# Kernel optimization log

Hardware: AMD Instinct MI355X
Metric: run time of the kernel (lower is better)

The kernel has to match this reference:

```python
import jax, jax.numpy as jnp
import numpy as np

N, E, G = 50000, 800000, 64
IN, HID, T, EDGE_DIM, HLS = 32, 64, 2, 2, 32
# deg histogram: all nodes degree 16 -> avg_deg['log'] = log(16+1)
AVG_LOG = float(np.log(17.0))


def _pna(x, src, dst, eattr, We, be, Wpre, bpre, Wpost, bpost, Wlin, blin):
    """PNAConv with aggregators [mean,min,max,std], scalers [identity,amp,att],
    towers=T, pre_layers=1, post_layers=1, divide_input=False."""
    n, F = x.shape
    enc = eattr @ We + be                                   # [E, F] edge encoder
    # message: concat(x_i, x_j, edge) -> per-tower Linear(3F -> F)
    h = jnp.concatenate([x[dst], x[src], enc], axis=-1)     # [E, 3F] (same for all towers)
    m = jnp.einsum('ef,tfo->eto', h, Wpre) + bpre           # [E, T, F]
    ones = jnp.ones((m.shape[0],), m.dtype)
    cnt = jax.ops.segment_sum(ones, dst, num_segments=n)    # in-degree [N]
    d = jnp.maximum(cnt, 1.0)[:, None, None]
    s = jax.ops.segment_sum(m, dst, num_segments=n)
    mean = s / d
    msq = jax.ops.segment_sum(m * m, dst, num_segments=n) / d
    std = jnp.sqrt(jax.nn.relu(msq - mean * mean) + 1e-5)
    has = (cnt > 0)[:, None, None]
    mn = jnp.where(has, jax.ops.segment_min(m, dst, num_segments=n), 0.0)
    mx = jnp.where(has, jax.ops.segment_max(m, dst, num_segments=n), 0.0)
    agg = jnp.concatenate([mean, mn, mx, std], axis=-1)     # [N, T, 4F]
    logd = jnp.log(d + 1.0)
    scaled = jnp.concatenate([agg, agg * (logd / AVG_LOG), agg * (AVG_LOG / logd)], axis=-1)  # [N,T,12F]
    xt = jnp.broadcast_to(x[:, None, :], (n, Wpre.shape[0], F))
    out = jnp.concatenate([xt, scaled], axis=-1)            # [N, T, 13F]
    o = jnp.einsum('nti,tio->nto', out, Wpost) + bpost      # [N, T, F_out]
    return o.reshape(n, -1) @ Wlin + blin                   # [N, HID]


def setup_inputs():
    key = jax.random.key(0)
    ks = iter(jax.random.split(key, 48))
    def p(shape):
        return jax.random.normal(next(ks), shape, jnp.float32) * 0.05
    inp = {}
    inp['x'] = jax.random.normal(next(ks), (N, IN), jnp.float32)
    inp['edge_attr'] = jax.random.normal(next(ks), (E, EDGE_DIM), jnp.float32)
    inp['hls_attr'] = jax.random.normal(next(ks), (G, HLS), jnp.float32)
    inp['edge_index'] = jax.random.randint(next(ks), (2, E), 0, N)
    inp['batch'] = jnp.sort(jax.random.randint(next(ks), (N,), 0, G))
    Fo = HID // T
    for l, Fin in enumerate([IN, HID]):
        inp[f'We{l}'] = p((EDGE_DIM, Fin)); inp[f'be{l}'] = jnp.zeros((Fin,), jnp.float32)
        inp[f'Wpre{l}'] = p((T, 3 * Fin, Fin)); inp[f'bpre{l}'] = jnp.zeros((T, Fin), jnp.float32)
        inp[f'Wpost{l}'] = p((T, 13 * Fin, Fo)); inp[f'bpost{l}'] = jnp.zeros((T, Fo), jnp.float32)
        inp[f'Wlin{l}'] = p((HID, HID)); inp[f'blin{l}'] = jnp.zeros((HID,), jnp.float32)
    inp['W1'] = p((HID + HLS, 64)); inp['b1'] = jnp.zeros((64,), jnp.float32)
    inp['W2'] = p((64, 64)); inp['b2'] = jnp.zeros((64,), jnp.float32)
    inp['W3'] = p((64, 1)); inp['b3'] = jnp.zeros((1,), jnp.float32)
    return inp


def reference(x, edge_attr, hls_attr,
              We0, be0, Wpre0, bpre0, Wpost0, bpost0, Wlin0, blin0,
              We1, be1, Wpre1, bpre1, Wpost1, bpost1, Wlin1, blin1,
              W1, b1, W2, b2, W3, b3,
              edge_index, batch):
    src, dst = edge_index[0], edge_index[1]
    h = jax.nn.relu(_pna(x, src, dst, edge_attr, We0, be0, Wpre0, bpre0, Wpost0, bpost0, Wlin0, blin0))
    h = jax.nn.relu(_pna(h, src, dst, edge_attr, We1, be1, Wpre1, bpre1, Wpost1, bpost1, Wlin1, blin1))
    g = jax.ops.segment_sum(h, batch, num_segments=G)       # global_add_pool [G, HID]
    g = jnp.concatenate([g, hls_attr], axis=-1)
    g = jax.nn.relu(g @ W1 + b1)
    g = jax.nn.relu(g @ W2 + b2)
    return g @ W3 + b3                                      # [G, 1]
```

## Files before the change

### kernel.cpp

```cpp
#include <hip/hip_runtime.h>
#include <math.h>
#include <float.h>

#define NN 50000
#define EE 800000
#define CAP 64

#define NB 196
#define SPAN 256
#define BCAP 4608

typedef unsigned short ushort_t;
typedef short short8 __attribute__((ext_vector_type(8)));
typedef float floatx4 __attribute__((ext_vector_type(4)));

__device__ __constant__ float kAVG_LOG = 2.8332133440562162f;

__device__ inline ushort_t f2bf(float v) {
    union { float f; unsigned u; } x; x.f = v;
    unsigned r = x.u + 0x7fffu + ((x.u >> 16) & 1u);
    return (ushort_t)(r >> 16);
}
__device__ inline float bf2f(ushort_t b) {
    union { unsigned u; float f; } x; x.u = ((unsigned)b) << 16; return x.f;
}
__device__ inline float bitsf(unsigned u) {
    union { unsigned u; float f; } x; x.u = u; return x.f;
}
__device__ inline void splitbf(float v, ushort_t& hi, ushort_t& lo) {
    hi = f2bf(v);
    lo = f2bf(v - bf2f(hi));
}

template <int F>
__device__ void prep_ab_dev(const float* __restrict__ We, const float* __restrict__ be,
                            const float* __restrict__ Wpre, const float* __restrict__ bpre,
                            float* __restrict__ U, float* __restrict__ Wab,
                            float* __restrict__ bias_ab) {
    const int TF = 2 * F;
    int tid = threadIdx.x;
    for (int idx = tid; idx < 2 * TF; idx += 1024) {
        int c = idx / TF, f = idx % TF;
        int t = f / F, o = f % F;
        float s = 0.f;
        for (int g = 0; g < F; ++g)
            s += We[c * F + g] * Wpre[((size_t)t * 3 * F + 2 * F + g) * F + o];
        U[idx] = s;
    }
    for (int idx = tid; idx < F * 2 * TF; idx += 1024) {
        int g = idx / (2 * TF), cc = idx % (2 * TF);
        int t, o, row;
        if (cc < TF) { t = cc / F; o = cc % F; row = g; }
        else { int c2 = cc - TF; t = c2 / F; o = c2 % F; row = F + g; }
        Wab[idx] = Wpre[((size_t)t * 3 * F + row) * F + o];
    }
    for (int cc = tid; cc < 2 * TF; cc += 1024) {
        float v = 0.f;
        if (cc < TF) {
            int t = cc / F, o = cc % F;
            float s = 0.f;
            for (int g = 0; g < F; ++g)
                s += be[g] * Wpre[((size_t)t * 3 * F + 2 * F + g) * F + o];
            v = s + bpre[t * F + o];
        }
        bias_ab[cc] = v;
    }
}

template <int F>
__device__ void prep_zf_elem(int idx, const float* __restrict__ Wpost, const float* __restrict__ Wlin,
                             ushort_t* __restrict__ Bh, ushort_t* __restrict__ Bl) {
    const int KT = 9 * F;
    int jg = idx / KT, k = idx - jg * KT;
    int b = jg >> 6, j = jg & 63;
    float v = 0.f;
    if (k < F) {
        if (b == 0) {
#pragma unroll
            for (int t = 0; t < 2; ++t)
#pragma unroll
                for (int c = 0; c < 32; ++c)
                    v += Wpost[((size_t)t * 13 * F + k) * 32 + c] * Wlin[(t * 32 + c) * 64 + j];
        }
    } else {
        int r = k - F;
        int t = r / (4 * F), rr = r - t * 4 * F;
#pragma unroll
        for (int c = 0; c < 32; ++c)
            v += Wpost[((size_t)t * 13 * F + F + b * 4 * F + rr) * 32 + c] * Wlin[(t * 32 + c) * 64 + j];
    }
    ushort_t h_, l_;
    splitbf(v, h_, l_);
    Bh[(size_t)jg * KT + k] = h_;
    Bl[(size_t)jg * KT + k] = l_;
}

#define PARTB 196
#define PZ0B  54
#define PZ1B  108
#define PINITB 1563

__global__ __launch_bounds__(1024) void prep_part_init(
    const int* __restrict__ ei, const float* __restrict__ ea,
    int* __restrict__ gcount, uint2* __restrict__ part,
    const float* We0, const float* be0, const float* Wpre0, const float* bpre0,
    const float* Wpost0, const float* Wlin0, const float* bpost0, const float* blin0,
    const float* We1, const float* be1, const float* Wpre1, const float* bpre1,
    const float* Wpost1, const float* Wlin1, const float* bpost1, const float* blin1,
    float* U0, float* Wab0, float* bias_ab0, ushort_t* Bh0, ushort_t* Bl0, float* bias_zf0,
    float* U1, float* Wab1, float* bias_ab1, ushort_t* Bh1, ushort_t* Bl1, float* bias_zf1,
    const float* __restrict__ x, ushort_t* __restrict__ xb) {
    __shared__ int hist[NB];
    __shared__ int lbase[NB];
    int tid = threadIdx.x;
    int b = blockIdx.x;
    if (b < PARTB) {
        int e0 = b * 4096;
        for (int i = tid; i < NB; i += 1024) hist[i] = 0;
        __syncthreads();
        int bq[4], rnk[4];
        unsigned px[4], py[4];
#pragma unroll
        for (int q = 0; q < 4; ++q) {
            int e = e0 + q * 1024 + tid;
            bq[q] = -1;
            if (e < EE) {
                int s = ei[e];
                int d = ei[EE + e];
                float2 v = *(const float2*)(ea + 2 * e);
                bq[q] = d >> 8;
                px[q] = ((unsigned)(d & 255) << 16) | (unsigned)s;
                py[q] = ((unsigned)f2bf(v.y) << 16) | (unsigned)f2bf(v.x);
                rnk[q] = atomicAdd(&hist[bq[q]], 1);
            }
        }
        __syncthreads();
        for (int i = tid; i < NB; i += 1024)
            lbase[i] = atomicAdd(&gcount[i], hist[i]);
        __syncthreads();
#pragma unroll
        for (int q = 0; q < 4; ++q) {
            if (bq[q] >= 0) {
                int slot = lbase[bq[q]] + rnk[q];
                if (slot < BCAP)
                    part[(size_t)bq[q] * BCAP + slot] = make_uint2(px[q], py[q]);
            }
        }
        return;
    }
    b -= PARTB;
    if (b < PZ0B) {
        prep_zf_elem<32>(b * 1024 + tid, Wpost0, Wlin0, Bh0, Bl0);
    } else if (b < PZ0B + PZ1B) {
        prep_zf_elem<64>((b - PZ0B) * 1024 + tid, Wpost1, Wlin1, Bh1, Bl1);
    } else if (b == PZ0B + PZ1B) {
        prep_ab_dev<32>(We0, be0, Wpre0, bpre0, U0, Wab0, bias_ab0);
    } else if (b == PZ0B + PZ1B + 1) {
        prep_ab_dev<64>(We1, be1, Wpre1, bpre1, U1, Wab1, bias_ab1);
    } else if (b == PZ0B + PZ1B + 2) {
        for (int j = tid; j < 64; j += 1024) {
            float s0 = blin0[j], s1 = blin1[j];
#pragma unroll
            for (int t = 0; t < 2; ++t)
#pragma unroll
                for (int c = 0; c < 32; ++c) {
                    s0 += bpost0[t * 32 + c] * Wlin0[(t * 32 + c) * 64 + j];
                    s1 += bpost1[t * 32 + c] * Wlin1[(t * 32 + c) * 64 + j];
                }
            bias_zf0[j] = s0;
            bias_zf1[j] = s1;
        }
    } else {
        int i = (b - (PZ0B + PZ1B + 3)) * 1024 + tid;
        if (i < NN * 32) xb[i] = f2bf(x[i]);
    }
}

__device__ void csr_fill_block(int g, const int* __restrict__ gcount,
                               const uint2* __restrict__ part,
                               int* __restrict__ cnt, uint2* __restrict__ csr) {
    __shared__ int lcnt[SPAN];
    int tid = threadIdx.x;
    lcnt[tid] = 0;
    __syncthreads();
    int total = gcount[g];
    if (total > BCAP) total = BCAP;
    size_t pbase = (size_t)g * BCAP;
    for (int i = tid; i < total; i += 256) {
        uint2 rec = part[pbase + i];
        int rel = rec.x >> 16;
        int src = rec.x & 0xffff;
        int p = atomicAdd(&lcnt[rel], 1);
        if (p < CAP) {
            int node = (g << 8) + rel;
            csr[(size_t)node * CAP + p] = make_uint2((unsigned)src, rec.y);
        }
    }
    __syncthreads();
    int node = (g << 8) + tid;
    if (node < NN) cnt[node] = lcnt[tid];
}

__device__ void gemm_bias_block(const float* __restrict__ A, const float* __restrict__ B,
                                const float* __restrict__ bias, float* __restrict__ Ca,
                                ushort_t* __restrict__ Cb, int M, int K, int Ncols, int bstart,
                                int mb, int cb) {
    __shared__ float As[32][132];
    __shared__ float Bs[32][68];
    int m0 = mb * 128, c0 = cb * 64;
    int tid = threadIdx.x;
    int tx = tid & 15, ty = tid >> 4;
    int ms = tid >> 3, u = tid & 7;
    float acc[8][4] = {};
    for (int k0 = 0; k0 < K; k0 += 32) {
#pragma unroll
        for (int p = 0; p < 4; ++p) {
            int m = ms + 32 * p;
            int gm = m0 + m;
            float4 v = make_float4(0.f, 0.f, 0.f, 0.f);
            if (gm < M) v = *(const float4*)(A + (size_t)gm * K + k0 + u * 4);
            As[u * 4 + 0][m] = v.x; As[u * 4 + 1][m] = v.y;
            As[u * 4 + 2][m] = v.z; As[u * 4 + 3][m] = v.w;
        }
#pragma unroll
        for (int p = 0; p < 2; ++p) {
            int idx = tid + 256 * p;
            int kk = idx >> 4, q = idx & 15;
            *(float4*)&Bs[kk][q * 4] = *(const float4*)(B + (size_t)(k0 + kk) * Ncols + c0 + q * 4);
        }
        __syncthreads();
#pragma unroll 8
        for (int k = 0; k < 32; ++k) {
            float a0[8], b0[4];
            *(float4*)&a0[0] = *(const float4*)&As[k][ty * 8];
            *(float4*)&a0[4] = *(const float4*)&As[k][ty * 8 + 4];
            *(float4*)&b0[0] = *(const float4*)&Bs[k][tx * 4];
#pragma unroll
            for (int i = 0; i < 8; ++i)
#pragma unroll
                for (int j = 0; j < 4; ++j) acc[i][j] = fmaf(a0[i], b0[j], acc[i][j]);
        }
        __syncthreads();
    }
    float bj[4];
#pragma unroll
    for (int j = 0; j < 4; ++j) bj[j] = bias[c0 + tx * 4 + j];
    bool bside = (c0 >= bstart);
    int TFw = bstart;
#pragma unroll
    for (int i = 0; i < 8; ++i) {
        int gm = m0 + ty * 8 + i;
        if (gm >= M) continue;
        float v0 = acc[i][0] + bj[0], v1 = acc[i][1] + bj[1];
        float v2 = acc[i][2] + bj[2], v3 = acc[i][3] + bj[3];
        if (!bside) {
            *(float4*)(Ca + (size_t)gm * TFw + c0 + tx * 4) = make_float4(v0, v1, v2, v3);
        } else {
            ushort4 w;
            w.x = f2bf(v0); w.y = f2bf(v1); w.z = f2bf(v2); w.w = f2bf(v3);
            *(ushort4*)(Cb + (size_t)gm * TFw + (c0 - bstart) + tx * 4) = w;
        }
    }
}

__global__ __launch_bounds__(256) void gemm_bias(const float* __restrict__ A, const float* __restrict__ B,
                                                 const float* __restrict__ bias, float* __restrict__ Ca,
                                                 ushort_t* __restrict__ Cb, int M, int K, int Ncols, int bstart) {
    gemm_bias_block(A, B, bias, Ca, Cb, M, K, Ncols, bstart, blockIdx.x, blockIdx.y);
}

__global__ __launch_bounds__(256) void csr_gemm0(
    const int* __restrict__ gcount, const uint2* __restrict__ part,
    int* __restrict__ cnt, uint2* __restrict__ csr,
    const float* __restrict__ A, const float* __restrict__ B, const float* __restrict__ bias,
    float* __restrict__ Ca, ushort_t* __restrict__ Cb) {
    int bx = blockIdx.x;
    if (bx % 5 == 0) {
        csr_fill_block(bx / 5, gcount, part, cnt, csr);
    } else {
        int idx = bx - 1 - bx / 5;
        gemm_bias_block(A, B, bias, Ca, Cb, NN, 32, 128, 64, idx % 391, idx / 391);
    }
}

template <int F>
__global__ __launch_bounds__(256) void aggregate(const float* __restrict__ ABa, const ushort_t* __restrict__ ABb,
                                                 const int* __restrict__ cnt, const uint2* __restrict__ csr,
                                                 const float* __restrict__ U,
                                                 ushort_t* __restrict__ agg_b, float2* __restrict__ sc) {
    const int TF = 2 * F;
    const int FPL = TF / 64;
    int lane = threadIdx.x & 63;
    int n = blockIdx.x * 4 + (threadIdx.x >> 6);
    if (n >= NN) return;
    n = __builtin_amdgcn_readfirstlane(n);
    int f0 = FPL * lane;

    float base[FPL], u0[FPL], u1[FPL], sum[FPL], sq[FPL], mn[FPL], mx[FPL];
#pragma unroll
    for (int r = 0; r < FPL; ++r) {
        base[r] = ABa[(size_t)n * TF + f0 + r];
        u0[r] = U[f0 + r];
        u1[r] = U[TF + f0 + r];
        sum[r] = 0.f; sq[r] = 0.f; mn[r] = FLT_MAX; mx[r] = -FLT_MAX;
    }
    int deg = cnt[n];
    int ec = deg < CAP ? deg : CAP;
    const uint2* __restrict__ p = csr + (size_t)n * CAP;

    auto body = [&](unsigned epi, unsigned wvi) {
        float ex = bitsf(epi << 16);
        float ey = bitsf(epi & 0xffff0000u);
        float v[FPL];
        if constexpr (FPL == 2) {
            v[0] = bitsf(wvi << 16);
            v[1] = bitsf(wvi & 0xffff0000u);
        } else {
            v[0] = bitsf(wvi << 16);
        }
#pragma unroll
        for (int r = 0; r < FPL; ++r) {
            float q = fmaf(ex, u0[r], fmaf(ey, u1[r], v[r]));
            sum[r] += q;
            sq[r] = fmaf(q, q, sq[r]);
            mn[r] = fminf(mn[r], q);
            mx[r] = fmaxf(mx[r], q);
        }
    };

    for (int e0 = 0; e0 < ec; e0 += 16) {
        uint4 c[8];
#pragma unroll
        for (int j = 0; j < 8; ++j) c[j] = *(const uint4*)(p + e0 + 2 * j);
        unsigned sb[16], ep[16];
#pragma unroll
        for (int j = 0; j < 8; ++j) {
            sb[2 * j] = c[j].x;     ep[2 * j] = c[j].y;
            sb[2 * j + 1] = c[j].z; ep[2 * j + 1] = c[j].w;
        }
        int rem = ec - e0;
        unsigned wv[16];
        if (rem >= 16) {
#pragma unroll
            for (int i = 0; i < 16; ++i) {
                const ushort_t* row = ABb + (size_t)sb[i] * TF;
                if constexpr (FPL == 2) wv[i] = *(const unsigned*)(row + f0);
                else wv[i] = row[f0];
            }
#pragma unroll
            for (int i = 0; i < 16; ++i) body(ep[i], wv[i]);
        } else {
#pragma unroll
            for (int i = 0; i < 16; ++i) {
                if (i < rem) {
                    const ushort_t* row = ABb + (size_t)sb[i] * TF;
                    if constexpr (FPL == 2) wv[i] = *(const unsigned*)(row + f0);
                    else wv[i] = row[f0];
                }
            }
#pragma unroll
            for (int i = 0; i < 16; ++i)
                if (i < rem) body(ep[i], wv[i]);
        }
    }

    float d = (float)(deg > 1 ? deg : 1);
    float inv_d = 1.f / d;
    bool has = deg > 0;
#pragma unroll
    for (int r = 0; r < FPL; ++r) {
        float mean_q = sum[r] * inv_d;
        float var = sq[r] * inv_d - mean_q * mean_q;
        float stdv = sqrtf(fmaxf(var, 0.f) + 1e-5f);
        float mean = has ? base[r] + mean_q : 0.f;
        float vmn = has ? base[r] + mn[r] : 0.f;
        float vmx = has ? base[r] + mx[r] : 0.f;
        int f = f0 + r;
        int t = f / F, o = f - t * F;
        size_t rowb = (size_t)n * (4 * TF) + (size_t)t * (4 * F);
        agg_b[rowb + o] = f2bf(mean);
        agg_b[rowb + F + o] = f2bf(vmn);
        agg_b[rowb + 2 * F + o] = f2bf(vmx);
        agg_b[rowb + 3 * F + o] = f2bf(stdv);
    }
    if (lane == 0) {
        float logd = logf(d + 1.f);
        sc[n] = make_float2(logd / kAVG_LOG, kAVG_LOG / logd);
    }
}

template <int F, bool POOL>
__global__ __launch_bounds__(512, 2) void gemm_zf(
    const ushort_t* __restrict__ xs_b, const ushort_t* __restrict__ agg_b,
    const ushort_t* __restrict__ Bh, const ushort_t* __restrict__ Bl,
    const float* __restrict__ bias_zf, const float2* __restrict__ sc,
    float* __restrict__ H, ushort_t* __restrict__ H_b,
    const int* __restrict__ batch, float* __restrict__ pool) {
    const int KT = 9 * F;
    extern __shared__ char smem[];
    ushort_t* A_s  = (ushort_t*)smem;
    ushort_t* Bh_s = A_s + 128 * 40;
    ushort_t* Bl_s = Bh_s + 192 * 40;
    float* hbuf = (float*)smem;

    int m0 = blockIdx.x * 128;
    int tid = threadIdx.x;
    int lane = tid & 63;
    int wave = tid >> 6;
    int wr = wave >> 2;
    int wc = wave & 3;
    int ln = lane & 15, quad = lane >> 4;

    floatx4 acc[4][3];
#pragma unroll
    for (int i = 0; i < 4; ++i)
#pragma unroll
        for (int j = 0; j < 3; ++j) acc[i][j] = (floatx4)(0.f);

    int arow = tid >> 2, asg = tid & 3;
    int bcol[2], bsg[2];
    bool bok[2];
#pragma unroll
    for (int p = 0; p < 2; ++p) {
        int idx = tid + 512 * p;
        bok[p] = idx < 768;
        bcol[p] = idx >> 2;
        bsg[p] = idx & 3;
    }

    const short8 zero8 = {0, 0, 0, 0, 0, 0, 0, 0};
    short8 pa, pbh[2], pbl[2];
    {
        int c0 = asg * 8;
        int gm = m0 + arow;
        pa = zero8;
        if (gm < NN) pa = *(const short8*)(xs_b + (size_t)gm * F + c0);
#pragma unroll
        for (int p = 0; p < 2; ++p) {
            pbh[p] = zero8; pbl[p] = zero8;
            if (bok[p]) {
                pbh[p] = *(const short8*)(Bh + (size_t)bcol[p] * KT + bsg[p] * 8);
                pbl[p] = *(const short8*)(Bl + (size_t)bcol[p] * KT + bsg[p] * 8);
            }
        }
    }

    for (int k0 = 0; k0 < KT; k0 += 32) {
        *(short8*)&A_s[arow * 40 + asg * 8] = pa;
#pragma unroll
        for (int p = 0; p < 2; ++p) {
            if (bok[p]) {
                *(short8*)&Bh_s[bcol[p] * 40 + bsg[p] * 8] = pbh[p];
                *(short8*)&Bl_s[bcol[p] * 40 + bsg[p] * 8] = pbl[p];
            }
        }
        __syncthreads();
        short8 bh[3], bl[3];
#pragma unroll
        for (int b = 0; b < 3; ++b) {
            int col = b * 64 + wc * 16 + ln;
            bh[b] = *(short8*)&Bh_s[col * 40 + quad * 8];
            bl[b] = *(short8*)&Bl_s[col * 40 + quad * 8];
        }
        int kn = k0 + 32;
        if (kn < KT) {
            int c0 = kn + asg * 8;
            int gm = m0 + arow;
            pa = zero8;
            if (gm < NN) {
                pa = (c0 < F) ? *(const short8*)(xs_b + (size_t)gm * F + c0)
                              : *(const short8*)(agg_b + (size_t)gm * 8 * F + (c0 - F));
            }
#pragma unroll
            for (int p = 0; p < 2; ++p) {
                if (bok[p]) {
                    pbh[p] = *(const short8*)(Bh + (size_t)bcol[p] * KT + kn + bsg[p] * 8);
                    pbl[p] = *(const short8*)(Bl + (size_t)bcol[p] * KT + kn + bsg[p] * 8);
                }
            }
        }
#pragma unroll
        for (int rf = 0; rf < 4; ++rf) {
            short8 ah = *(short8*)&A_s[((wr * 4 + rf) * 16 + ln) * 40 + quad * 8];
#pragma unroll
            for (int b = 0; b < 3; ++b) {
                acc[rf][b] = __builtin_amdgcn_mfma_f32_16x16x32_bf16(ah, bh[b], acc[rf][b], 0, 0, 0);
                acc[rf][b] = __builtin_amdgcn_mfma_f32_16x16x32_bf16(ah, bl[b], acc[rf][b], 0, 0, 0);
            }
        }
        __syncthreads();
    }

    int ocol = wc * 16 + ln;
    float bcolv = bias_zf[ocol];

    if (POOL) __syncthreads();

#pragma unroll
    for (int rf = 0; rf < 4; ++rf) {
#pragma unroll
        for (int reg = 0; reg < 4; ++reg) {
            int r = (wr * 4 + rf) * 16 + quad * 4 + reg;
            int gm = m0 + r;
            float2 s = make_float2(0.f, 0.f);
            if (gm < NN) s = sc[gm];
            float y = acc[rf][0][reg] + s.x * acc[rf][1][reg] + s.y * acc[rf][2][reg] + bcolv;
            y = fmaxf(y, 0.f);
            if (POOL) {
                hbuf[r * 68 + ocol] = (gm < NN) ? y : 0.f;
            } else if (gm < NN) {
                H[(size_t)gm * 64 + ocol] = y;
                H_b[(size_t)gm * 64 + ocol] = f2bf(y);
            }
        }
    }
    if (POOL) {
        __syncthreads();
        int col = tid & 63, grp = tid >> 6;
        float a = 0.f;
        int cur = -1;
        for (int i = 0; i < 16; ++i) {
            int r = grp * 16 + i;
            int gm = m0 + r;
            if (gm >= NN) break;
            int b = batch[gm];
            if (b != cur) {
                if (cur >= 0) atomicAdd(&pool[cur * 64 + col], a);
                cur = b; a = 0.f;
            }
            a += hbuf[r * 68 + col];
        }
        if (cur >= 0) atomicAdd(&pool[cur * 64 + col], a);
    }
}

__global__ __launch_bounds__(256) void head_kernel(const float* __restrict__ gpool, const float* __restrict__ hls,
                                                   const float* __restrict__ W1, const float* __restrict__ b1,
                                                   const float* __restrict__ W2, const float* __restrict__ b2,
                                                   const float* __restrict__ W3, const float* __restrict__ b3,
                                                   float* __restrict__ out) {
    __shared__ float gin[64][96];
    __shared__ float r1[64][64];
    __shared__ float r2[64][64];
    int tid = threadIdx.x;
    for (int idx = tid; idx < 64 * 96; idx += 256) {
        int g = idx / 96, j = idx % 96;
        gin[g][j] = (j < 64) ? gpool[g * 64 + j] : hls[g * 32 + (j - 64)];
    }
    __syncthreads();
    for (int idx = tid; idx < 64 * 64; idx += 256) {
        int g = idx / 64, j = idx % 64;
        float acc = b1[j];
        for (int k = 0; k < 96; ++k) acc = fmaf(gin[g][k], W1[k * 64 + j], acc);
        r1[g][j] = fmaxf(acc, 0.f);
    }
    __syncthreads();
    for (int idx = tid; idx < 64 * 64; idx += 256) {
        int g = idx / 64, j = idx % 64;
        float acc = b2[j];
        for (int k = 0; k < 64; ++k) acc = fmaf(r1[g][k], W2[k * 64 + j], acc);
        r2[g][j] = fmaxf(acc, 0.f);
    }
    __syncthreads();
    if (tid < 64) {
        float acc = b3[0];
        for (int k = 0; k < 64; ++k) acc = fmaf(r2[tid][k], W3[k], acc);
        out[tid] = acc;
    }
}

extern "C" void kernel_launch(void* const* d_in, const int* in_sizes, int n_in,
                              void* d_out, int out_size, void* d_ws, size_t ws_size,
                              hipStream_t stream) {
    (void)in_sizes; (void)n_in; (void)out_size; (void)ws_size;
    const float* x     = (const float*)d_in[0];
    const float* eattr = (const float*)d_in[1];
    const float* hls   = (const float*)d_in[2];
    const int*   eidx  = (const int*)d_in[3];
    const int*   batch = (const int*)d_in[4];
    const float* We[2]    = {(const float*)d_in[5],  (const float*)d_in[13]};
    const float* be[2]    = {(const float*)d_in[6],  (const float*)d_in[14]};
    const float* Wpre[2]  = {(const float*)d_in[7],  (const float*)d_in[15]};
    const float* bpre[2]  = {(const float*)d_in[8],  (const float*)d_in[16]};
    const float* Wpost[2] = {(const float*)d_in[9],  (const float*)d_in[17]};
    const float* bpost[2] = {(const float*)d_in[10], (const float*)d_in[18]};
    const float* Wlin[2]  = {(const float*)d_in[11], (const float*)d_in[19]};
    const float* blin[2]  = {(const float*)d_in[12], (const float*)d_in[20]};
    const float* W1 = (const float*)d_in[21]; const float* b1 = (const float*)d_in[22];
    const float* W2 = (const float*)d_in[23]; const float* b2 = (const float*)d_in[24];
    const float* W3 = (const float*)d_in[25]; const float* b3 = (const float*)d_in[26];
    float* out = (float*)d_out;

    char* ws = (char*)d_ws;
    size_t off = 0;
    auto carve = [&](size_t bytes) -> char* {
        char* p = ws + off;
        off = (off + bytes + 255) & ~(size_t)255;
        return p;
    };
    int*      cnt      = (int*)carve((size_t)NN * 4);
    uint2*    csr      = (uint2*)carve((size_t)NN * CAP * 8);
    float*    ABa      = (float*)carve((size_t)NN * 128 * 4);
    ushort_t* ABb      = (ushort_t*)carve((size_t)NN * 128 * 2);
    ushort_t* agg_b    = (ushort_t*)carve((size_t)NN * 512 * 2);
    float2*   sc       = (float2*)carve((size_t)NN * 8);
    ushort_t* xs_b     = (ushort_t*)carve((size_t)NN * 32 * 2);
    float*    h1       = (float*)carve((size_t)NN * 64 * 4);
    ushort_t* h1_b     = (ushort_t*)carve((size_t)NN * 64 * 2);
    float*    U0       = (float*)carve(256 * 4);
    float*    U1       = (float*)carve(256 * 4);
    float*    Wab0     = (float*)carve(16384 * 4);
    float*    Wab1     = (float*)carve(16384 * 4);
    float*    bias_ab0 = (float*)carve(256 * 4);
    float*    bias_ab1 = (float*)carve(256 * 4);
    ushort_t* Bh0      = (ushort_t*)carve((size_t)192 * 288 * 2);
    ushort_t* Bl0      = (ushort_t*)carve((size_t)192 * 288 * 2);
    ushort_t* Bh1      = (ushort_t*)carve((size_t)192 * 576 * 2);
    ushort_t* Bl1      = (ushort_t*)carve((size_t)192 * 576 * 2);
    float*    bias_zf0 = (float*)carve(64 * 4);
    float*    bias_zf1 = (float*)carve(64 * 4);
    float*    pool     = (float*)carve(64 * 64 * 4);
    int*      gcount   = (int*)carve(NB * 4);
    uint2*    part     = (uint2*)agg_b;

    const int MB128 = (NN + 127) / 128;
    const int SMEM_ZF = (128 * 40 + 192 * 40 + 192 * 40) * 2;
    const int FUSEDB = NB + MB128 * 2;
    const int MERGEDB = PARTB + PZ0B + PZ1B + 3 + PINITB;

    hipMemsetAsync(gcount, 0, NB * 4, stream);
    hipMemsetAsync(pool, 0, 64 * 64 * 4, stream);

    prep_part_init<<<MERGEDB, 1024, 0, stream>>>(
        eidx, eattr, gcount, part,
        We[0], be[0], Wpre[0], bpre[0], Wpost[0], Wlin[0], bpost[0], blin[0],
        We[1], be[1], Wpre[1], bpre[1], Wpost[1], Wlin[1], bpost[1], blin[1],
        U0, Wab0, bias_ab0, Bh0, Bl0, bias_zf0,
        U1, Wab1, bias_ab1, Bh1, Bl1, bias_zf1,
        x, xs_b);

    csr_gemm0<<<FUSEDB, 256, 0, stream>>>(gcount, part, cnt, csr, x, Wab0, bias_ab0, ABa, ABb);
    aggregate<32><<<(NN + 3) / 4, 256, 0, stream>>>(ABa, ABb, cnt, csr, U0, agg_b, sc);
    gemm_zf<32, false><<<MB128, 512, SMEM_ZF, stream>>>(xs_b, agg_b, Bh0, Bl0, bias_zf0, sc,
                                                        h1, h1_b, batch, pool);

    gemm_bias<<<dim3(MB128, 4), 256, 0, stream>>>(h1, Wab1, bias_ab1, ABa, ABb, NN, 64, 256, 128);
    aggregate<64><<<(NN + 3) / 4, 256, 0, stream>>>(ABa, ABb, cnt, csr, U1, agg_b, sc);
    gemm_zf<64, true><<<MB128, 512, SMEM_ZF, stream>>>(h1_b, agg_b, Bh1, Bl1, bias_zf1, sc,
                                                       nullptr, nullptr, batch, pool);

    head_kernel<<<1, 256, 0, stream>>>(pool, hls, W1, b1, W2, b2, W3, b3, out);
}
```

Before: 321.5 us.

## Fuse neighbor aggregation into the post-GEMM kernel per 128-row tile

Removes the standalone aggregate kernel launches. Each 512-thread GEMM block now first aggregates its own 128 nodes, one wave per node over 16 passes, writing agg_b and sc. It then syncs and runs the existing post-transform GEMM on those rows. This saves a launch and kernel boundary per layer and may keep the aggregated rows in cache, but aggregation now runs at the GEMM kernel's lower grid size and occupancy (launch_bounds 512,2), which can reduce latency hiding for the irregular gathers.

```diff
diff --git a/kernel.cpp b/kernel.cpp
--- a/kernel.cpp
+++ b/kernel.cpp
@@ -284,15 +284,13 @@
 }
 
 template <int F>
-__global__ __launch_bounds__(256) void aggregate(const float* __restrict__ ABa, const ushort_t* __restrict__ ABb,
-                                                 const int* __restrict__ cnt, const uint2* __restrict__ csr,
-                                                 const float* __restrict__ U,
-                                                 ushort_t* __restrict__ agg_b, float2* __restrict__ sc) {
+__device__ void agg_node(int n, int lane,
+                         const float* __restrict__ ABa, const ushort_t* __restrict__ ABb,
+                         const int* __restrict__ cnt, const uint2* __restrict__ csr,
+                         const float* __restrict__ U,
+                         ushort_t* agg_b, float2* sc) {
     const int TF = 2 * F;
     const int FPL = TF / 64;
-    int lane = threadIdx.x & 63;
-    int n = blockIdx.x * 4 + (threadIdx.x >> 6);
-    if (n >= NN) return;
     n = __builtin_amdgcn_readfirstlane(n);
     int f0 = FPL * lane;
 
@@ -390,10 +388,13 @@
 }
 
 template <int F, bool POOL>
-__global__ __launch_bounds__(512, 2) void gemm_zf(
-    const ushort_t* __restrict__ xs_b, const ushort_t* __restrict__ agg_b,
+__global__ __launch_bounds__(512, 2) void aggzf(
+    const float* __restrict__ ABa, const ushort_t* __restrict__ ABb,
+    const int* __restrict__ cnt, const uint2* __restrict__ csr,
+    const float* __restrict__ U,
+    const ushort_t* __restrict__ xs_b, ushort_t* agg_b,
     const ushort_t* __restrict__ Bh, const ushort_t* __restrict__ Bl,
-    const float* __restrict__ bias_zf, const float2* __restrict__ sc,
+    const float* __restrict__ bias_zf, float2* sc,
     float* __restrict__ H, ushort_t* __restrict__ H_b,
     const int* __restrict__ batch, float* __restrict__ pool) {
     const int KT = 9 * F;
@@ -407,6 +408,15 @@
     int tid = threadIdx.x;
     int lane = tid & 63;
     int wave = tid >> 6;
+
+#pragma unroll 1
+    for (int pss = 0; pss < 16; ++pss) {
+        int n = m0 + pss * 8 + wave;
+        if (n < NN)
+            agg_node<F>(n, lane, ABa, ABb, cnt, csr, U, agg_b, sc);
+    }
+    __syncthreads();
+
     int wr = wave >> 2;
     int wc = wave & 3;
     int ln = lane & 15, quad = lane >> 4;
@@ -640,14 +650,14 @@
         x, xs_b);
 
     csr_gemm0<<<FUSEDB, 256, 0, stream>>>(gcount, part, cnt, csr, x, Wab0, bias_ab0, ABa, ABb);
-    aggregate<32><<<(NN + 3) / 4, 256, 0, stream>>>(ABa, ABb, cnt, csr, U0, agg_b, sc);
-    gemm_zf<32, false><<<MB128, 512, SMEM_ZF, stream>>>(xs_b, agg_b, Bh0, Bl0, bias_zf0, sc,
-                                                        h1, h1_b, batch, pool);
+    aggzf<32, false><<<MB128, 512, SMEM_ZF, stream>>>(
+        ABa, ABb, cnt, csr, U0, xs_b, agg_b, Bh0, Bl0, bias_zf0, sc,
+        h1, h1_b, batch, pool);
 
     gemm_bias<<<dim3(MB128, 4), 256, 0, stream>>>(h1, Wab1, bias_ab1, ABa, ABb, NN, 64, 256, 128);
-    aggregate<64><<<(NN + 3) / 4, 256, 0, stream>>>(ABa, ABb, cnt, csr, U1, agg_b, sc);
-    gemm_zf<64, true><<<MB128, 512, SMEM_ZF, stream>>>(h1_b, agg_b, Bh1, Bl1, bias_zf1, sc,
-                                                       nullptr, nullptr, batch, pool);
+    aggzf<64, true><<<MB128, 512, SMEM_ZF, stream>>>(
+        ABa, ABb, cnt, csr, U1, h1_b, agg_b, Bh1, Bl1, bias_zf1, sc,
+        nullptr, nullptr, batch, pool);
 
     head_kernel<<<1, 256, 0, stream>>>(pool, hls, W1, b1, W2, b2, W3, b3, out);
 }
```

Result: slower. 340.4 us (+5.9%).
